# Kernel optimization log

Measured on AMD Instinct MI355X. Metric: run time of the kernel, lower is better.

## Reference

```python
import jax, jax.numpy as jnp
import numpy as np

N, NFEAT, NHID, NREL, NCLASS, NHEADS = 4096, 512, 64, 64, 16, 8
ALPHA = 0.2   # LeakyReLU negative slope
NEG = -9e15   # pyGAT mask value


def _gat_layer(x, rel, mask, adj_ad, W, a1, a2, concat):
    # x: [N, Fin], rel: [nrel, Fin], mask: [N, N] bool, adj_ad: [N, nrel]
    xr = x + adj_ad @ rel                 # relation-augmented node features
    h = xr @ W                            # [N, Fout]
    f1 = h @ a1                           # [N]  (a^T[Wh_i||Wh_j] = f1_i + f2_j)
    f2 = h @ a2                           # [N]
    e = jax.nn.leaky_relu(f1[:, None] + f2[None, :], ALPHA)  # [N, N]
    att = jax.nn.softmax(jnp.where(mask, e, NEG), axis=1)
    out = att @ h                         # [N, Fout]
    return jax.nn.elu(out) if concat else out


def setup_inputs() -> dict:
    key = jax.random.key(0)
    ks = jax.random.split(key, 12)
    x = jax.random.normal(ks[0], (N, NFEAT), jnp.float32)
    rel = jax.random.normal(ks[1], (NREL, NFEAT), jnp.float32)
    rel_dict = jax.random.randint(ks[2], (N,), 0, NREL, jnp.int32)
    adj = (jax.random.uniform(ks[3], (N, N)) < 0.01).astype(jnp.float32)
    adj = jnp.maximum(adj, jnp.eye(N, dtype=jnp.float32))  # self loops
    adj_ad = jax.random.uniform(ks[4], (N, NREL), jnp.float32)
    adj_ad = adj_ad / adj_ad.sum(axis=1, keepdims=True)
    s_in = 1.0 / np.sqrt(NFEAT)
    s_hid = 1.0 / np.sqrt(NHID)
    s_cat = 1.0 / np.sqrt(NHID * NHEADS)
    W_heads = jax.random.normal(ks[5], (NHEADS, NFEAT, NHID), jnp.float32) * s_in
    a1_heads = jax.random.normal(ks[6], (NHEADS, NHID), jnp.float32) * s_hid
    a2_heads = jax.random.normal(ks[7], (NHEADS, NHID), jnp.float32) * s_hid
    W_out = jax.random.normal(ks[8], (NHID * NHEADS, NFEAT), jnp.float32) * s_cat
    a1_out = jax.random.normal(ks[9], (NFEAT,), jnp.float32) * s_in
    a2_out = jax.random.normal(ks[10], (NFEAT,), jnp.float32) * s_in
    lin_W = jax.random.normal(ks[11], (NFEAT, NCLASS), jnp.float32) * s_in
    lin_b = jnp.zeros((NCLASS,), jnp.float32)
    return {"x": x, "rel": rel, "rel_dict": rel_dict, "adj": adj, "adj_ad": adj_ad,
            "W_heads": W_heads, "a1_heads": a1_heads, "a2_heads": a2_heads,
            "W_out": W_out, "a1_out": a1_out, "a2_out": a2_out,
            "lin_W": lin_W, "lin_b": lin_b}


def reference(x, rel, rel_dict, adj, adj_ad, W_heads, a1_heads, a2_heads,
              W_out, a1_out, a2_out, lin_W, lin_b):
    # dropout is identity at inference (training=False); rel_dict is only used
    # by the repo to build adj/adj_ad, so it is a non-math constant here.
    mask = adj > 0
    # multi-head GAT layer, heads fused via vmap then concatenated on feature dim
    heads = jax.vmap(lambda W, a1, a2: _gat_layer(x, rel, mask, adj_ad, W, a1, a2, True))(
        W_heads, a1_heads, a2_heads)                      # [H, N, NHID]
    hcat = jnp.moveaxis(heads, 0, 1).reshape(N, NHEADS * NHID)  # [N, H*NHID]
    h2 = _gat_layer(hcat, rel, mask, adj_ad, W_out, a1_out, a2_out, False)  # [N, NFEAT]
    logits = jax.nn.elu(h2 @ lin_W + lin_b)               # [N, NCLASS]
    return jax.nn.log_softmax(logits, axis=1)
```

## Files before the change

kernel.cpp:

```cpp
#include <hip/hip_runtime.h>

#define NN      4096
#define FEAT    512
#define KDIM    576
#define NHID    64
#define NHEADS  8
#define NCLS    16
#define MAXDEG  128
#define ALPHA   0.2f

typedef __bf16 bf16_t;
typedef __bf16 bf16x8_t __attribute__((ext_vector_type(8)));
typedef float  f32x4_t  __attribute__((ext_vector_type(4)));
typedef unsigned short us8_t __attribute__((ext_vector_type(8)));

__device__ inline unsigned short f2bf(float f) {
    unsigned int u = __float_as_uint(f);
    u += 0x7fffu + ((u >> 16) & 1u);
    return (unsigned short)(u >> 16);
}
__device__ inline float bfu2f(unsigned short b) {
    return __uint_as_float(((unsigned int)b) << 16);
}

#define PREP_REL0   0
#define PREP_TR0    256
#define PREP_Z0     384
#define PREP_CAST0  392
#define PREP_CSR0   2440
#define PREP_NBLK   3464

__global__ __launch_bounds__(256) void prep_kernel(
    const float* __restrict__ adj, int* __restrict__ deg, int* __restrict__ cols,
    const float* __restrict__ adj_ad, const float* __restrict__ rel,
    const float* __restrict__ x, bf16_t* __restrict__ Abf,
    bf16_t* __restrict__ Abf2,
    const float* __restrict__ Wh, const float* __restrict__ Wo,
    unsigned short* __restrict__ WcT, unsigned short* __restrict__ WoT,
    float* __restrict__ f1o, float* __restrict__ f2o) {
    int b = blockIdx.x;
    int t = threadIdx.x;
    __shared__ float smem[64 * 65];
    if (b < PREP_TR0) {
        int r  = b & 63;
        int nh = (b >> 6) & 1;
        int n  = nh * 256 + t;
        smem[t]       = rel[r * FEAT + t];
        smem[t + 256] = rel[r * FEAT + 256 + t];
        __syncthreads();
        float acc[8] = {};
        if (b < 128) {
            int h = n >> 6, f = n & 63;
            const float* p = Wh + (size_t)h * 32768 + f;
            for (int k0 = 0; k0 < 512; k0 += 8)
                #pragma unroll
                for (int u = 0; u < 8; ++u)
                    acc[u] += smem[k0 + u] * p[(size_t)(k0 + u) * 64];
            float s = ((acc[0] + acc[1]) + (acc[2] + acc[3]))
                    + ((acc[4] + acc[5]) + (acc[6] + acc[7]));
            WcT[(size_t)n * KDIM + 512 + r] = f2bf(s);
        } else {
            const float* p = Wo + n;
            for (int k0 = 0; k0 < 512; k0 += 8)
                #pragma unroll
                for (int u = 0; u < 8; ++u)
                    acc[u] += smem[k0 + u] * p[(size_t)(k0 + u) * 512];
            float s = ((acc[0] + acc[1]) + (acc[2] + acc[3]))
                    + ((acc[4] + acc[5]) + (acc[6] + acc[7]));
            WoT[(size_t)n * KDIM + 512 + r] = f2bf(s);
        }
    } else if (b < PREP_Z0) {
        int tb = b - PREP_TR0;
        if (tb < 64) {
            int h = tb >> 3, k0 = (tb & 7) * 64;
            const float* src = Wh + (size_t)h * 32768 + (size_t)k0 * 64;
            #pragma unroll
            for (int i2 = 0; i2 < 16; ++i2) {
                int li = t + i2 * 256;
                float v = src[li];
                smem[(li & 63) * 65 + (li >> 6)] = v;
            }
            __syncthreads();
            #pragma unroll
            for (int i2 = 0; i2 < 16; ++i2) {
                int li = t + i2 * 256;
                int f = li >> 6, r = li & 63;
                WcT[(size_t)(h * 64 + f) * KDIM + k0 + r] = f2bf(smem[f * 65 + r]);
            }
        } else {
            int wb = tb - 64;
            int n0 = (wb & 7) * 64, k0 = (wb >> 3) * 64;
            #pragma unroll
            for (int i2 = 0; i2 < 16; ++i2) {
                int li = t + i2 * 256;
                int r = li >> 6, f = li & 63;
                float v = Wo[(size_t)(k0 + r) * 512 + n0 + f];
                smem[f * 65 + r] = v;
            }
            __syncthreads();
            #pragma unroll
            for (int i2 = 0; i2 < 16; ++i2) {
                int li = t + i2 * 256;
                int f = li >> 6, r = li & 63;
                WoT[(size_t)(n0 + f) * KDIM + k0 + r] = f2bf(smem[f * 65 + r]);
            }
        }
    } else if (b < PREP_CAST0) {
        int g = (b - PREP_Z0) * 256 + t;
        if (g < 1024) ((float4*)f1o)[g] = make_float4(0.f, 0.f, 0.f, 0.f);
        else ((float4*)f2o)[g - 1024] = make_float4(0.f, 0.f, 0.f, 0.f);
    } else if (b < PREP_CSR0) {
        int half = t >> 7;
        int tt = t & 127;
        size_t i = (size_t)(b - PREP_CAST0) * 2 + half;
        float4 xv = ((const float4*)(x + i * FEAT))[tt];
        ushort4 o;
        o.x = f2bf(xv.x); o.y = f2bf(xv.y);
        o.z = f2bf(xv.z); o.w = f2bf(xv.w);
        *(ushort4*)(Abf + i * KDIM + 4 * tt) = o;
        if (tt < 16) {
            float4 av = ((const float4*)(adj_ad + i * 64))[tt];
            ushort4 o2;
            o2.x = f2bf(av.x); o2.y = f2bf(av.y);
            o2.z = f2bf(av.z); o2.w = f2bf(av.w);
            *(ushort4*)(Abf  + i * KDIM + 512 + 4 * tt) = o2;
            *(ushort4*)(Abf2 + i * KDIM + 512 + 4 * tt) = o2;
        }
    } else {
        int l = t & 63;
        int i = (b - PREP_CSR0) * 4 + (t >> 6);
        const float4* row4 = (const float4*)(adj + (size_t)i * NN);
        float4 v[16];
        #pragma unroll
        for (int c2 = 0; c2 < 16; ++c2) v[c2] = row4[l + c2 * 64];
        unsigned long long mask = 0;
        #pragma unroll
        for (int c2 = 0; c2 < 16; ++c2) {
            unsigned m4 = (unsigned)(v[c2].x > 0.0f)
                        | ((unsigned)(v[c2].y > 0.0f) << 1)
                        | ((unsigned)(v[c2].z > 0.0f) << 2)
                        | ((unsigned)(v[c2].w > 0.0f) << 3);
            mask |= (unsigned long long)m4 << (4 * c2);
        }
        int c = __popcll(mask);
        int pre = c;
        #pragma unroll
        for (int off = 1; off < 64; off <<= 1) {
            int n = __shfl_up(pre, off);
            if (l >= off) pre += n;
        }
        int base = pre - c;
        if (l == 63) deg[i] = pre > MAXDEG ? MAXDEG : pre;
        int* colrow = cols + i * MAXDEG;
        int idx = base;
        while (mask) {
            int bit = (int)__ffsll(mask) - 1;
            mask &= mask - 1;
            int j = 4 * l + ((bit >> 2) << 8) + (bit & 3);
            if (idx < MAXDEG) colrow[idx] = j;
            ++idx;
        }
    }
}

__global__ __launch_bounds__(256) void gemm_bf16_dot_kernel(
    const bf16_t* __restrict__ A, const bf16_t* __restrict__ Bt,
    unsigned short* __restrict__ Cbf,
    const float* __restrict__ a1, const float* __restrict__ a2,
    float* __restrict__ f1, float* __restrict__ f2, int layer2) {
    __shared__ __align__(16) bf16_t As[64][72];
    __shared__ __align__(16) bf16_t Bs[64][72];
    const int bm = blockIdx.x * 64;
    const int bn = blockIdx.y * 64;
    const int t  = threadIdx.x;
    const int lr = t >> 3;
    const int lc = (t & 7) * 8;
    const int l  = t & 63;
    const int w  = t >> 6;
    const int mrow = w * 16 + (l & 15);
    const int nrow = l & 15;
    const int q8 = (l >> 4) * 8;

    const bf16_t* Ap0 = A  + (size_t)(bm + lr)      * KDIM + lc;
    const bf16_t* Ap1 = A  + (size_t)(bm + 32 + lr) * KDIM + lc;
    const bf16_t* Bp0 = Bt + (size_t)(bn + lr)      * KDIM + lc;
    const bf16_t* Bp1 = Bt + (size_t)(bn + 32 + lr) * KDIM + lc;
    uint4 ra0 = *(const uint4*)(Ap0);
    uint4 ra1 = *(const uint4*)(Ap1);
    uint4 rb0 = *(const uint4*)(Bp0);
    uint4 rb1 = *(const uint4*)(Bp1);

    f32x4_t acc[4] = {};
    for (int k0 = 0; k0 < KDIM; k0 += 64) {
        *(uint4*)&As[lr][lc]      = ra0;
        *(uint4*)&As[32 + lr][lc] = ra1;
        *(uint4*)&Bs[lr][lc]      = rb0;
        *(uint4*)&Bs[32 + lr][lc] = rb1;
        __syncthreads();
        if (k0 + 64 < KDIM) {
            ra0 = *(const uint4*)(Ap0 + k0 + 64);
            ra1 = *(const uint4*)(Ap1 + k0 + 64);
            rb0 = *(const uint4*)(Bp0 + k0 + 64);
            rb1 = *(const uint4*)(Bp1 + k0 + 64);
        }
        #pragma unroll
        for (int kk = 0; kk < 64; kk += 32) {
            bf16x8_t a = *(const bf16x8_t*)&As[mrow][kk + q8];
            #pragma unroll
            for (int nt = 0; nt < 4; ++nt) {
                bf16x8_t b = *(const bf16x8_t*)&Bs[nt * 16 + nrow][kk + q8];
                acc[nt] = __builtin_amdgcn_mfma_f32_16x16x32_bf16(a, b, acc[nt], 0, 0, 0);
            }
        }
        __syncthreads();
    }
    const int crow = bm + w * 16 + (l >> 4) * 4;
    const int ccol = bn + (l & 15);
    #pragma unroll
    for (int nt = 0; nt < 4; ++nt)
        #pragma unroll
        for (int r = 0; r < 4; ++r)
            Cbf[(size_t)(crow + r) * FEAT + ccol + nt * 16] = f2bf(acc[nt][r]);

    float a1v[4], a2v[4];
    #pragma unroll
    for (int nt = 0; nt < 4; ++nt) {
        a1v[nt] = a1[bn + (l & 15) + nt * 16];
        a2v[nt] = a2[bn + (l & 15) + nt * 16];
    }
    float p1[4] = {}, p2[4] = {};
    #pragma unroll
    for (int nt = 0; nt < 4; ++nt)
        #pragma unroll
        for (int r = 0; r < 4; ++r) {
            p1[r] += acc[nt][r] * a1v[nt];
            p2[r] += acc[nt][r] * a2v[nt];
        }
    #pragma unroll
    for (int off = 1; off <= 8; off <<= 1)
        #pragma unroll
        for (int r = 0; r < 4; ++r) {
            p1[r] += __shfl_xor(p1[r], off);
            p2[r] += __shfl_xor(p2[r], off);
        }
    if ((l & 15) == 0) {
        int row = bm + w * 16 + (l >> 4) * 4;
        if (layer2) {
            #pragma unroll
            for (int r = 0; r < 4; ++r) {
                atomicAdd(&f1[row + r], p1[r]);
                atomicAdd(&f2[row + r], p2[r]);
            }
        } else {
            #pragma unroll
            for (int r = 0; r < 4; ++r) {
                f1[blockIdx.y * NN + row + r] = p1[r];
                f2[blockIdx.y * NN + row + r] = p2[r];
            }
        }
    }
}

__global__ __launch_bounds__(512) void att1_kernel(
    const bf16_t* __restrict__ Hbf, const float* __restrict__ f1,
    const float* __restrict__ f2, const int* __restrict__ deg,
    const int* __restrict__ cols, bf16_t* __restrict__ outbf) {
    int i = blockIdx.x;
    int tid = threadIdx.x;
    int h = tid >> 6;
    int l = tid & 63;
    __shared__ int jl[MAXDEG];
    __shared__ float se[NHEADS][MAXDEG];
    __shared__ float part[NHEADS][FEAT];
    __shared__ float sinv[NHEADS];
    __shared__ int sdeg;
    if (tid == 0) sdeg = deg[i];
    __syncthreads();
    int d = sdeg;
    int dpad = (d + 31) & ~31;
    for (int k = tid; k < dpad; k += 512)
        jl[k] = (k < d) ? cols[i * MAXDEG + k] : i;
    __syncthreads();
    float fi = f1[h * NN + i];
    float lmax = -1e30f;
    for (int k = l; k < d; k += 64) {
        float e = fi + f2[h * NN + jl[k]];
        e = e > 0.0f ? e : ALPHA * e;
        se[h][k] = e;
        lmax = fmaxf(lmax, e);
    }
    for (int off = 32; off; off >>= 1) lmax = fmaxf(lmax, __shfl_down(lmax, off));
    float m = __shfl(lmax, 0);
    float ls = 0.0f;
    for (int k = l; k < d; k += 64) {
        float p = __expf(se[h][k] - m);
        se[h][k] = p;
        ls += p;
    }
    for (int k = d + l; k < dpad; k += 64) se[h][k] = 0.0f;
    for (int off = 32; off; off >>= 1) ls += __shfl_down(ls, off);
    if (l == 0) sinv[h] = 1.0f / ls;
    __syncthreads();
    const int myhead = l >> 3;
    float acc[8] = {};
    for (int k0 = 0; k0 < dpad; k0 += 32) {
        float pw[4];
        const bf16_t* rp[4];
        #pragma unroll
        for (int j = 0; j < 4; ++j) {
            int k = k0 + j * 8 + h;
            pw[j] = se[myhead][k];
            rp[j] = Hbf + (size_t)jl[k] * FEAT + l * 8;
        }
        #pragma unroll
        for (int j = 0; j < 4; ++j) {
            us8_t v = *(const us8_t*)rp[j];
            float p = pw[j];
            #pragma unroll
            for (int q = 0; q < 8; ++q) acc[q] += p * bfu2f(v[q]);
        }
    }
    *(float4*)&part[h][l * 8]     = make_float4(acc[0], acc[1], acc[2], acc[3]);
    *(float4*)&part[h][l * 8 + 4] = make_float4(acc[4], acc[5], acc[6], acc[7]);
    __syncthreads();
    {
        float sum = 0.0f;
        #pragma unroll
        for (int w2 = 0; w2 < NHEADS; ++w2) sum += part[w2][tid];
        float o = sum * sinv[tid >> 6];
        o = o > 0.0f ? o : __expf(o) - 1.0f;
        ((unsigned short*)outbf)[(size_t)i * KDIM + tid] = f2bf(o);
    }
}

__global__ __launch_bounds__(256) void att2_final_kernel(
    const bf16_t* __restrict__ Hbf, const float* __restrict__ f1,
    const float* __restrict__ f2, const int* __restrict__ deg,
    const int* __restrict__ cols, const float* __restrict__ linW,
    const float* __restrict__ linb, float* __restrict__ out) {
    int i = blockIdx.x;
    int t = threadIdx.x;
    __shared__ int jl[MAXDEG];
    __shared__ float sp[MAXDEG];
    __shared__ float red[4];
    __shared__ float part[3][FEAT];
    __shared__ float hrow[FEAT];
    __shared__ float clsred[16][NCLS];
    __shared__ float sl[NCLS];
    __shared__ int sdeg;
    if (t == 0) sdeg = deg[i];
    __syncthreads();
    int d = sdeg;
    int dpad = (d + 15) & ~15;
    if (t < dpad) jl[t] = (t < d) ? cols[i * MAXDEG + t] : i;
    __syncthreads();
    float e = 0.0f, lmax = -1e30f;
    if (t < d) {
        e = f1[i] + f2[jl[t]];
        e = e > 0.0f ? e : ALPHA * e;
        lmax = e;
    }
    for (int off = 32; off; off >>= 1) lmax = fmaxf(lmax, __shfl_down(lmax, off));
    if ((t & 63) == 0) red[t >> 6] = lmax;
    __syncthreads();
    float m = fmaxf(fmaxf(red[0], red[1]), fmaxf(red[2], red[3]));
    float p = 0.0f;
    if (t < d) p = __expf(e - m);
    if (t < dpad) sp[t] = p;
    float ls = p;
    for (int off = 32; off; off >>= 1) ls += __shfl_down(ls, off);
    __syncthreads();
    if ((t & 63) == 0) red[t >> 6] = ls;
    __syncthreads();
    float s = red[0] + red[1] + red[2] + red[3];
    float inv = 1.0f / s;
    const int slot = t >> 6;
    const int cg   = t & 63;
    float acc[8] = {};
    for (int k0 = 0; k0 < dpad; k0 += 16) {
        float pw[4];
        const bf16_t* rp[4];
        #pragma unroll
        for (int j = 0; j < 4; ++j) {
            int k = k0 + j * 4 + slot;
            pw[j] = sp[k];
            rp[j] = Hbf + (size_t)jl[k] * FEAT + cg * 8;
        }
        #pragma unroll
        for (int j = 0; j < 4; ++j) {
            us8_t v = *(const us8_t*)rp[j];
            float pk = pw[j];
            #pragma unroll
            for (int q = 0; q < 8; ++q) acc[q] += pk * bfu2f(v[q]);
        }
    }
    if (slot > 0) {
        float* dst = &part[slot - 1][cg * 8];
        *(float4*)(dst)     = make_float4(acc[0], acc[1], acc[2], acc[3]);
        *(float4*)(dst + 4) = make_float4(acc[4], acc[5], acc[6], acc[7]);
    }
    __syncthreads();
    if (slot == 0) {
        #pragma unroll
        for (int sl2 = 0; sl2 < 3; ++sl2)
            #pragma unroll
            for (int j = 0; j < 8; ++j) acc[j] += part[sl2][cg * 8 + j];
        float* dst = &hrow[cg * 8];
        *(float4*)(dst)     = make_float4(acc[0] * inv, acc[1] * inv, acc[2] * inv, acc[3] * inv);
        *(float4*)(dst + 4) = make_float4(acc[4] * inv, acc[5] * inv, acc[6] * inv, acc[7] * inv);
    }
    __syncthreads();
    {
        int c = t & 15;
        int seg = t >> 4;
        float partial = 0.0f;
        int f0 = seg * 32;
        #pragma unroll 8
        for (int f = f0; f < f0 + 32; ++f) partial += hrow[f] * linW[f * NCLS + c];
        clsred[seg][c] = partial;
    }
    __syncthreads();
    if (t < NCLS) {
        float logit = linb[t];
        #pragma unroll
        for (int seg = 0; seg < 16; ++seg) logit += clsred[seg][t];
        logit = logit > 0.0f ? logit : __expf(logit) - 1.0f;
        sl[t] = logit;
    }
    __syncthreads();
    if (t < NCLS) {
        float mm = sl[0];
        #pragma unroll
        for (int c = 1; c < NCLS; ++c) mm = fmaxf(mm, sl[c]);
        float ssum = 0.0f;
        #pragma unroll
        for (int c = 0; c < NCLS; ++c) ssum += __expf(sl[c] - mm);
        out[i * NCLS + t] = sl[t] - mm - logf(ssum);
    }
}

extern "C" void kernel_launch(void* const* d_in, const int* in_sizes, int n_in,
                              void* d_out, int out_size, void* d_ws, size_t ws_size,
                              hipStream_t stream) {
    const float* x        = (const float*)d_in[0];
    const float* rel      = (const float*)d_in[1];
    const float* adj      = (const float*)d_in[3];
    const float* adj_ad   = (const float*)d_in[4];
    const float* W_heads  = (const float*)d_in[5];
    const float* a1_heads = (const float*)d_in[6];
    const float* a2_heads = (const float*)d_in[7];
    const float* W_out    = (const float*)d_in[8];
    const float* a1_out   = (const float*)d_in[9];
    const float* a2_out   = (const float*)d_in[10];
    const float* lin_W    = (const float*)d_in[11];
    const float* lin_b    = (const float*)d_in[12];
    float* out = (float*)d_out;

    char* ws = (char*)d_ws;
    bf16_t* Abf  = (bf16_t*)(ws);
    bf16_t* Abf2 = (bf16_t*)(ws + (5u  << 20));
    bf16_t* Hbf1 = (bf16_t*)(ws + (10u << 20));
    bf16_t* Hbf2 = (bf16_t*)(ws + (14u << 20));
    bf16_t* WcT  = (bf16_t*)(ws + (18u << 20));
    bf16_t* WoT  = (bf16_t*)(ws + (19u << 20));
    float*  f1   = (float*) (ws + (20u << 20));
    float*  f2   = (float*) (ws + (20u << 20) + (128u << 10));
    float*  f1o  = (float*) (ws + (20u << 20) + (256u << 10));
    float*  f2o  = (float*) (ws + (20u << 20) + (272u << 10));
    int*    deg  = (int*)   (ws + (20u << 20) + (288u << 10));
    int*    cols = (int*)   (ws + (21u << 20));

    prep_kernel<<<PREP_NBLK, 256, 0, stream>>>(
        adj, deg, cols, adj_ad, rel, x, Abf, Abf2, W_heads, W_out,
        (unsigned short*)WcT, (unsigned short*)WoT, f1o, f2o);
    gemm_bf16_dot_kernel<<<dim3(64, 8), 256, 0, stream>>>(
        Abf, WcT, (unsigned short*)Hbf1, a1_heads, a2_heads, f1, f2, 0);
    att1_kernel<<<NN, 512, 0, stream>>>(Hbf1, f1, f2, deg, cols, Abf2);
    gemm_bf16_dot_kernel<<<dim3(64, 8), 256, 0, stream>>>(
        Abf2, WoT, (unsigned short*)Hbf2, a1_out, a2_out, f1o, f2o, 1);
    att2_final_kernel<<<NN, 256, 0, stream>>>(Hbf2, f1o, f2o, deg, cols, lin_W, lin_b, out);
}
```

Baseline: 188.4 us.

## Enlarge GEMM tiles to 128x128 with direct-to-LDS loads; deepen gather unroll

The bf16 GEMM moves from 64x64 to 128x128 block tiles, with each wave computing a 4x4 grid of MFMA tiles. Tiles are loaded straight into LDS with global_load_lds instead of staging through registers, which drops the register-prefetch double buffering. The aim is more data reuse and fewer LDS round-trips per MFMA, but the grid shrinks to 128 blocks, which may leave CUs idle on a 256-CU part. The sparse-gather loops in both attention kernels are also unrolled twice as deep (8 rows in flight), at the cost of more padding rows.

```diff
diff --git a/kernel.cpp b/kernel.cpp
--- a/kernel.cpp
+++ b/kernel.cpp
@@ -21,6 +21,11 @@
 }
 __device__ inline float bfu2f(unsigned short b) {
     return __uint_as_float(((unsigned int)b) << 16);
+}
+__device__ inline void gload16(const void* g, void* s) {
+    __builtin_amdgcn_global_load_lds(
+        (const __attribute__((address_space(1))) void*)g,
+        (__attribute__((address_space(3))) void*)s, 16, 0, 0);
 }
 
 #define PREP_REL0   0
@@ -168,96 +173,106 @@
     unsigned short* __restrict__ Cbf,
     const float* __restrict__ a1, const float* __restrict__ a2,
     float* __restrict__ f1, float* __restrict__ f2, int layer2) {
-    __shared__ __align__(16) bf16_t As[64][72];
-    __shared__ __align__(16) bf16_t Bs[64][72];
-    const int bm = blockIdx.x * 64;
-    const int bn = blockIdx.y * 64;
+    __shared__ __align__(16) bf16_t As[128][64];
+    __shared__ __align__(16) bf16_t Bs[128][64];
+    const int bm = blockIdx.x * 128;
+    const int bn = blockIdx.y * 128;
+    const int by = blockIdx.y;
     const int t  = threadIdx.x;
-    const int lr = t >> 3;
-    const int lc = (t & 7) * 8;
     const int l  = t & 63;
     const int w  = t >> 6;
-    const int mrow = w * 16 + (l & 15);
-    const int nrow = l & 15;
-    const int q8 = (l >> 4) * 8;
-
-    const bf16_t* Ap0 = A  + (size_t)(bm + lr)      * KDIM + lc;
-    const bf16_t* Ap1 = A  + (size_t)(bm + 32 + lr) * KDIM + lc;
-    const bf16_t* Bp0 = Bt + (size_t)(bn + lr)      * KDIM + lc;
-    const bf16_t* Bp1 = Bt + (size_t)(bn + 32 + lr) * KDIM + lc;
-    uint4 ra0 = *(const uint4*)(Ap0);
-    uint4 ra1 = *(const uint4*)(Ap1);
-    uint4 rb0 = *(const uint4*)(Bp0);
-    uint4 rb1 = *(const uint4*)(Bp1);
-
-    f32x4_t acc[4] = {};
+    const int wr = w >> 1;
+    const int wc = w & 1;
+    const int c16 = l & 15;
+    const int q8  = (l >> 4) * 8;
+    const int r4  = (l >> 4) * 4;
+
+    const bf16_t* Abase = A  + (size_t)bm * KDIM;
+    const bf16_t* Bbase = Bt + (size_t)bn * KDIM;
+
+    f32x4_t acc[4][4] = {};
     for (int k0 = 0; k0 < KDIM; k0 += 64) {
-        *(uint4*)&As[lr][lc]      = ra0;
-        *(uint4*)&As[32 + lr][lc] = ra1;
-        *(uint4*)&Bs[lr][lc]      = rb0;
-        *(uint4*)&Bs[32 + lr][lc] = rb1;
+        #pragma unroll
+        for (int c = 0; c < 4; ++c) {
+            int cb = c * 256 + w * 64;
+            int li = cb + l;
+            gload16(Abase + (size_t)(li >> 3) * KDIM + k0 + (li & 7) * 8,
+                    (char*)&As[0][0] + cb * 16);
+        }
+        #pragma unroll
+        for (int c = 0; c < 4; ++c) {
+            int cb = c * 256 + w * 64;
+            int li = cb + l;
+            gload16(Bbase + (size_t)(li >> 3) * KDIM + k0 + (li & 7) * 8,
+                    (char*)&Bs[0][0] + cb * 16);
+        }
         __syncthreads();
-        if (k0 + 64 < KDIM) {
-            ra0 = *(const uint4*)(Ap0 + k0 + 64);
-            ra1 = *(const uint4*)(Ap1 + k0 + 64);
-            rb0 = *(const uint4*)(Bp0 + k0 + 64);
-            rb1 = *(const uint4*)(Bp1 + k0 + 64);
-        }
         #pragma unroll
         for (int kk = 0; kk < 64; kk += 32) {
-            bf16x8_t a = *(const bf16x8_t*)&As[mrow][kk + q8];
-            #pragma unroll
-            for (int nt = 0; nt < 4; ++nt) {
-                bf16x8_t b = *(const bf16x8_t*)&Bs[nt * 16 + nrow][kk + q8];
-                acc[nt] = __builtin_amdgcn_mfma_f32_16x16x32_bf16(a, b, acc[nt], 0, 0, 0);
-            }
+            bf16x8_t af[4], bfr[4];
+            #pragma unroll
+            for (int mi = 0; mi < 4; ++mi)
+                af[mi] = *(const bf16x8_t*)&As[wr * 64 + mi * 16 + c16][kk + q8];
+            #pragma unroll
+            for (int ni = 0; ni < 4; ++ni)
+                bfr[ni] = *(const bf16x8_t*)&Bs[wc * 64 + ni * 16 + c16][kk + q8];
+            #pragma unroll
+            for (int mi = 0; mi < 4; ++mi)
+                #pragma unroll
+                for (int ni = 0; ni < 4; ++ni)
+                    acc[mi][ni] = __builtin_amdgcn_mfma_f32_16x16x32_bf16(
+                        af[mi], bfr[ni], acc[mi][ni], 0, 0, 0);
         }
         __syncthreads();
     }
-    const int crow = bm + w * 16 + (l >> 4) * 4;
-    const int ccol = bn + (l & 15);
     #pragma unroll
-    for (int nt = 0; nt < 4; ++nt)
-        #pragma unroll
-        for (int r = 0; r < 4; ++r)
-            Cbf[(size_t)(crow + r) * FEAT + ccol + nt * 16] = f2bf(acc[nt][r]);
+    for (int mi = 0; mi < 4; ++mi)
+        #pragma unroll
+        for (int ni = 0; ni < 4; ++ni)
+            #pragma unroll
+            for (int r = 0; r < 4; ++r)
+                Cbf[(size_t)(bm + wr * 64 + mi * 16 + r4 + r) * FEAT
+                    + bn + wc * 64 + ni * 16 + c16] = f2bf(acc[mi][ni][r]);
 
     float a1v[4], a2v[4];
     #pragma unroll
-    for (int nt = 0; nt < 4; ++nt) {
-        a1v[nt] = a1[bn + (l & 15) + nt * 16];
-        a2v[nt] = a2[bn + (l & 15) + nt * 16];
-    }
-    float p1[4] = {}, p2[4] = {};
+    for (int ni = 0; ni < 4; ++ni) {
+        a1v[ni] = a1[bn + wc * 64 + ni * 16 + c16];
+        a2v[ni] = a2[bn + wc * 64 + ni * 16 + c16];
+    }
+    float p1[4][4] = {}, p2[4][4] = {};
     #pragma unroll
-    for (int nt = 0; nt < 4; ++nt)
-        #pragma unroll
-        for (int r = 0; r < 4; ++r) {
-            p1[r] += acc[nt][r] * a1v[nt];
-            p2[r] += acc[nt][r] * a2v[nt];
-        }
+    for (int mi = 0; mi < 4; ++mi)
+        #pragma unroll
+        for (int ni = 0; ni < 4; ++ni)
+            #pragma unroll
+            for (int r = 0; r < 4; ++r) {
+                p1[mi][r] += acc[mi][ni][r] * a1v[ni];
+                p2[mi][r] += acc[mi][ni][r] * a2v[ni];
+            }
     #pragma unroll
     for (int off = 1; off <= 8; off <<= 1)
         #pragma unroll
-        for (int r = 0; r < 4; ++r) {
-            p1[r] += __shfl_xor(p1[r], off);
-            p2[r] += __shfl_xor(p2[r], off);
-        }
-    if ((l & 15) == 0) {
-        int row = bm + w * 16 + (l >> 4) * 4;
-        if (layer2) {
+        for (int mi = 0; mi < 4; ++mi)
             #pragma unroll
             for (int r = 0; r < 4; ++r) {
-                atomicAdd(&f1[row + r], p1[r]);
-                atomicAdd(&f2[row + r], p2[r]);
-            }
-        } else {
+                p1[mi][r] += __shfl_xor(p1[mi][r], off);
+                p2[mi][r] += __shfl_xor(p2[mi][r], off);
+            }
+    if (c16 == 0) {
+        #pragma unroll
+        for (int mi = 0; mi < 4; ++mi)
             #pragma unroll
             for (int r = 0; r < 4; ++r) {
-                f1[blockIdx.y * NN + row + r] = p1[r];
-                f2[blockIdx.y * NN + row + r] = p2[r];
-            }
-        }
+                int row = bm + wr * 64 + mi * 16 + r4 + r;
+                if (layer2) {
+                    atomicAdd(&f1[row], p1[mi][r]);
+                    atomicAdd(&f2[row], p2[mi][r]);
+                } else {
+                    f1[(by * 2 + wc) * NN + row] = p1[mi][r];
+                    f2[(by * 2 + wc) * NN + row] = p2[mi][r];
+                }
+            }
     }
 }
 
@@ -277,7 +292,7 @@
     if (tid == 0) sdeg = deg[i];
     __syncthreads();
     int d = sdeg;
-    int dpad = (d + 31) & ~31;
+    int dpad = (d + 63) & ~63;
     for (int k = tid; k < dpad; k += 512)
         jl[k] = (k < d) ? cols[i * MAXDEG + k] : i;
     __syncthreads();
@@ -303,17 +318,17 @@
     __syncthreads();
     const int myhead = l >> 3;
     float acc[8] = {};
-    for (int k0 = 0; k0 < dpad; k0 += 32) {
-        float pw[4];
-        const bf16_t* rp[4];
-        #pragma unroll
-        for (int j = 0; j < 4; ++j) {
+    for (int k0 = 0; k0 < dpad; k0 += 64) {
+        float pw[8];
+        const bf16_t* rp[8];
+        #pragma unroll
+        for (int j = 0; j < 8; ++j) {
             int k = k0 + j * 8 + h;
             pw[j] = se[myhead][k];
             rp[j] = Hbf + (size_t)jl[k] * FEAT + l * 8;
         }
         #pragma unroll
-        for (int j = 0; j < 4; ++j) {
+        for (int j = 0; j < 8; ++j) {
             us8_t v = *(const us8_t*)rp[j];
             float p = pw[j];
             #pragma unroll
@@ -351,7 +366,7 @@
     if (t == 0) sdeg = deg[i];
     __syncthreads();
     int d = sdeg;
-    int dpad = (d + 15) & ~15;
+    int dpad = (d + 31) & ~31;
     if (t < dpad) jl[t] = (t < d) ? cols[i * MAXDEG + t] : i;
     __syncthreads();
     float e = 0.0f, lmax = -1e30f;
@@ -377,17 +392,17 @@
     const int slot = t >> 6;
     const int cg   = t & 63;
     float acc[8] = {};
-    for (int k0 = 0; k0 < dpad; k0 += 16) {
-        float pw[4];
-        const bf16_t* rp[4];
-        #pragma unroll
-        for (int j = 0; j < 4; ++j) {
+    for (int k0 = 0; k0 < dpad; k0 += 32) {
+        float pw[8];
+        const bf16_t* rp[8];
+        #pragma unroll
+        for (int j = 0; j < 8; ++j) {
             int k = k0 + j * 4 + slot;
             pw[j] = sp[k];
             rp[j] = Hbf + (size_t)jl[k] * FEAT + cg * 8;
         }
         #pragma unroll
-        for (int j = 0; j < 4; ++j) {
+        for (int j = 0; j < 8; ++j) {
             us8_t v = *(const us8_t*)rp[j];
             float pk = pw[j];
             #pragma unroll
@@ -473,10 +488,10 @@
     prep_kernel<<<PREP_NBLK, 256, 0, stream>>>(
         adj, deg, cols, adj_ad, rel, x, Abf, Abf2, W_heads, W_out,
         (unsigned short*)WcT, (unsigned short*)WoT, f1o, f2o);
-    gemm_bf16_dot_kernel<<<dim3(64, 8), 256, 0, stream>>>(
+    gemm_bf16_dot_kernel<<<dim3(32, 4), 256, 0, stream>>>(
         Abf, WcT, (unsigned short*)Hbf1, a1_heads, a2_heads, f1, f2, 0);
     att1_kernel<<<NN, 512, 0, stream>>>(Hbf1, f1, f2, deg, cols, Abf2);
-    gemm_bf16_dot_kernel<<<dim3(64, 8), 256, 0, stream>>>(
+    gemm_bf16_dot_kernel<<<dim3(32, 4), 256, 0, stream>>>(
         Abf2, WoT, (unsigned short*)Hbf2, a1_out, a2_out, f1o, f2o, 1);
     att2_final_kernel<<<NN, 256, 0, stream>>>(Hbf2, f1o, f2o, deg, cols, lin_W, lin_b, out);
 }
```

New measurement: 207.4 us. 10.1% more time.
